# Performance work log

Hardware: AMD Instinct MI355X
Metric: run time of the kernel (lower is better)

## Reference

```python
import jax, jax.numpy as jnp
import numpy as np

B, D_IN, C, P = 8192, 2048, 1000, 256


def setup_inputs() -> dict:
    key = jax.random.key(0)
    ks = jax.random.split(key, 6)
    return {
        "x": jax.random.normal(ks[0], (B, D_IN), dtype=jnp.float32),
        "Wm": jax.random.normal(ks[1], (C, D_IN), dtype=jnp.float32) * (1.0 / np.sqrt(D_IN)),
        "bm": jax.random.normal(ks[2], (C,), dtype=jnp.float32) * 0.01,
        "u": jax.random.normal(ks[3], (P, C), dtype=jnp.float32),
        "v": jax.random.normal(ks[4], (P, C), dtype=jnp.float32),
        "w": jax.random.normal(ks[5], (P, 1), dtype=jnp.float32),
    }


def reference(x, Wm, bm, u, v, w):
    # Backbone: Linear(D_IN -> C) producing per-instance logits (B, C)
    preds = jnp.einsum("bd,cd->bc", x, Wm) + bm
    # Gated attention, fully batched (replaces per-instance Python loop):
    # tanh(u @ pred) * sigmoid(v @ pred)  -> (B, P)
    gated = jnp.tanh(jnp.einsum("bc,pc->bp", preds, u)) * jax.nn.sigmoid(
        jnp.einsum("bc,pc->bp", preds, v)
    )
    scores = (gated @ w).ravel()          # (B,)
    attention = jax.nn.softmax(scores)    # softmax over instances
    total_pred = jnp.sum(preds * attention[:, None])
    return preds, total_pred
```

## Files before the change

### kernel.cpp

```cpp
#include <hip/hip_runtime.h>
#include <hip/hip_fp16.h>

typedef _Float16 half8 __attribute__((ext_vector_type(8)));
typedef float f32x4 __attribute__((ext_vector_type(4)));

#define B_   8192
#define DIN  2048
#define C_   1000
#define CP   1024
#define NP2  512

static const size_t OFF_XH  = 0;
static const size_t OFF_WH  = OFF_XH  + (size_t)B_ * DIN * 2;
static const size_t OFF_UVH = OFF_WH  + (size_t)CP * DIN * 2;
static const size_t OFF_PH  = OFF_UVH + (size_t)NP2 * CP * 2;
static const size_t OFF_SC  = OFF_PH  + (size_t)B_ * CP * 2;
static const size_t OFF_RS  = OFF_SC  + (size_t)B_ * 4;
static const size_t WS_NEED = OFF_RS  + (size_t)B_ * 4;

#define FENCE asm volatile("" ::: "memory")
#define BARRIER do { FENCE; __builtin_amdgcn_s_barrier(); FENCE; } while (0)
#define VMCNT(n) asm volatile("s_waitcnt vmcnt(" #n ")" ::: "memory")
#define PRIO1 __builtin_amdgcn_s_setprio(1)
#define PRIO0 __builtin_amdgcn_s_setprio(0)

__device__ __forceinline__ void gload16(const void* g, void* l) {
  __builtin_amdgcn_global_load_lds(
      (const __attribute__((address_space(1))) void*)g,
      (__attribute__((address_space(3))) void*)l, 16, 0, 0);
}

__global__ __launch_bounds__(256) void prep_kernel(
    const float* __restrict__ x, const float* __restrict__ Wm,
    const float* __restrict__ u, const float* __restrict__ v,
    _Float16* __restrict__ xh, _Float16* __restrict__ wh,
    _Float16* __restrict__ uvh, float* __restrict__ scores,
    float* __restrict__ rowsum)
{
  const long NX  = (long)B_ * DIN / 8;
  const long NW  = (long)CP * DIN / 8;
  const long NUV = (long)NP2 * CP / 8;
  const long NZ  = 2 * (long)B_ / 8;
  const long T   = NX + NW + NUV + NZ;
  for (long idx = (long)blockIdx.x * blockDim.x + threadIdx.x; idx < T;
       idx += (long)gridDim.x * blockDim.x) {
    if (idx < NX) {
      long e = idx * 8;
      float4 p0 = *(const float4*)(x + e);
      float4 p1 = *(const float4*)(x + e + 4);
      half8 h;
      h[0] = (_Float16)p0.x; h[1] = (_Float16)p0.y; h[2] = (_Float16)p0.z; h[3] = (_Float16)p0.w;
      h[4] = (_Float16)p1.x; h[5] = (_Float16)p1.y; h[6] = (_Float16)p1.z; h[7] = (_Float16)p1.w;
      *(half8*)(xh + e) = h;
    } else if (idx < NX + NW) {
      long e = (idx - NX) * 8;
      int row = (int)(e >> 11);
      half8 h;
      if (row < C_) {
        float4 p0 = *(const float4*)(Wm + e);
        float4 p1 = *(const float4*)(Wm + e + 4);
        h[0] = (_Float16)p0.x; h[1] = (_Float16)p0.y; h[2] = (_Float16)p0.z; h[3] = (_Float16)p0.w;
        h[4] = (_Float16)p1.x; h[5] = (_Float16)p1.y; h[6] = (_Float16)p1.z; h[7] = (_Float16)p1.w;
      } else {
        h = (half8)(_Float16)0.f;
      }
      *(half8*)(wh + e) = h;
    } else if (idx < NX + NW + NUV) {
      long e = (idx - NX - NW) * 8;
      int j = (int)(e >> 10);
      int k = (int)(e & 1023);
      const float* src = (j & 1) ? v : u;
      int p = j >> 1;
      half8 h;
      #pragma unroll
      for (int t = 0; t < 8; ++t) {
        int kk = k + t;
        h[t] = (kk < C_) ? (_Float16)src[(size_t)p * C_ + kk] : (_Float16)0.f;
      }
      *(half8*)(uvh + e) = h;
    } else {
      long e = (idx - NX - NW - NUV) * 8;
      float4 z = {0.f, 0.f, 0.f, 0.f};
      if (e < B_) {
        *(float4*)(scores + e) = z; *(float4*)(scores + e + 4) = z;
      } else {
        long r = e - B_;
        *(float4*)(rowsum + r) = z; *(float4*)(rowsum + r + 4) = z;
      }
    }
  }
}

__global__ __launch_bounds__(256, 1) void gemm1_kernel(
    const _Float16* __restrict__ xh, const _Float16* __restrict__ wh,
    const float* __restrict__ bmv, float* __restrict__ preds,
    _Float16* __restrict__ predsh, float* __restrict__ rowsum)
{
  __shared__ _Float16 lds[(3 * 32768 + 3 * 16384) / 2];
  char* const LB = (char*)lds;
  const int tid  = threadIdx.x;
  const int lane = tid & 63;
  const int w    = tid >> 6;
  const int wm   = w >> 1;
  const int wn   = w & 1;
  const int bm0  = blockIdx.x * 256;
  const int bn0  = blockIdx.y * 128;

  f32x4 acc[8][4] = {};

  const int trow = tid >> 3;
  const int swzc = (((tid & 7) << 4) ^ ((trow & 7) << 4)) >> 1;
  const _Float16* pA = xh + (size_t)(bm0 + trow) * DIN + swzc;
  const _Float16* pB = wh + (size_t)(bn0 + trow) * DIN + swzc;

  int aoff[8][2], boff[4][2];
  #pragma unroll
  for (int m = 0; m < 8; ++m)
    #pragma unroll
    for (int ks = 0; ks < 2; ++ks) {
      int ra = wm * 128 + m * 16 + (lane & 15);
      int kb = ks * 64 + (lane >> 4) * 16;
      aoff[m][ks] = ra * 128 + (kb ^ ((ra & 7) << 4));
    }
  #pragma unroll
  for (int n = 0; n < 4; ++n)
    #pragma unroll
    for (int ks = 0; ks < 2; ++ks) {
      int rb = wn * 64 + n * 16 + (lane & 15);
      int kb = ks * 64 + (lane >> 4) * 16;
      boff[n][ks] = rb * 128 + (kb ^ ((rb & 7) << 4));
    }

  half8 A[8][2], Bf[4][2];

  auto stA = [&](int c, int k) {
    gload16(pA + (size_t)k * 32 * DIN, LB + c * 32768 + k * 4096 + w * 1024);
  };
  auto stB = [&](int c, int k) {
    gload16(pB + (size_t)k * 32 * DIN, LB + 98304 + c * 16384 + k * 4096 + w * 1024);
  };
  auto advance = [&]() { pA += 64; pB += 64; };

  auto rdAL = [&](int c) {
    const char* b = LB + c * 32768;
    #pragma unroll
    for (int m = 0; m < 4; ++m)
      #pragma unroll
      for (int ks = 0; ks < 2; ++ks)
        A[m][ks] = *(const half8*)(b + aoff[m][ks]);
  };
  auto rdAH = [&](int c) {
    const char* b = LB + c * 32768;
    #pragma unroll
    for (int m = 4; m < 8; ++m)
      #pragma unroll
      for (int ks = 0; ks < 2; ++ks)
        A[m][ks] = *(const half8*)(b + aoff[m][ks]);
  };
  auto rdBL = [&](int c) {
    const char* b = LB + 98304 + c * 16384;
    #pragma unroll
    for (int n = 0; n < 2; ++n)
      #pragma unroll
      for (int ks = 0; ks < 2; ++ks)
        Bf[n][ks] = *(const half8*)(b + boff[n][ks]);
  };
  auto rdBH = [&](int c) {
    const char* b = LB + 98304 + c * 16384;
    #pragma unroll
    for (int n = 2; n < 4; ++n)
      #pragma unroll
      for (int ks = 0; ks < 2; ++ks)
        Bf[n][ks] = *(const half8*)(b + boff[n][ks]);
  };
  auto mfALBL = [&]() {
    #pragma unroll
    for (int m = 0; m < 4; ++m)
      #pragma unroll
      for (int n = 0; n < 2; ++n)
        #pragma unroll
        for (int ks = 0; ks < 2; ++ks)
          acc[m][n] = __builtin_amdgcn_mfma_f32_16x16x32_f16(A[m][ks], Bf[n][ks], acc[m][n], 0, 0, 0);
  };
  auto mfAHBL = [&]() {
    #pragma unroll
    for (int m = 4; m < 8; ++m)
      #pragma unroll
      for (int n = 0; n < 2; ++n)
        #pragma unroll
        for (int ks = 0; ks < 2; ++ks)
          acc[m][n] = __builtin_amdgcn_mfma_f32_16x16x32_f16(A[m][ks], Bf[n][ks], acc[m][n], 0, 0, 0);
  };
  auto mfALBH = [&]() {
    #pragma unroll
    for (int m = 0; m < 4; ++m)
      #pragma unroll
      for (int n = 2; n < 4; ++n)
        #pragma unroll
        for (int ks = 0; ks < 2; ++ks)
          acc[m][n] = __builtin_amdgcn_mfma_f32_16x16x32_f16(A[m][ks], Bf[n][ks], acc[m][n], 0, 0, 0);
  };
  auto mfAHBH = [&]() {
    #pragma unroll
    for (int m = 4; m < 8; ++m)
      #pragma unroll
      for (int n = 2; n < 4; ++n)
        #pragma unroll
        for (int ks = 0; ks < 2; ++ks)
          acc[m][n] = __builtin_amdgcn_mfma_f32_16x16x32_f16(A[m][ks], Bf[n][ks], acc[m][n], 0, 0, 0);
  };

  #pragma unroll
  for (int k = 0; k < 8; ++k) stA(0, k);
  #pragma unroll
  for (int k = 0; k < 4; ++k) stB(0, k);
  advance();
  #pragma unroll
  for (int k = 0; k < 8; ++k) stA(1, k);
  #pragma unroll
  for (int k = 0; k < 4; ++k) stB(1, k);
  advance();
  VMCNT(12);
  BARRIER;
  rdAL(0); rdBL(0);

  int c0 = 0;
  #pragma unroll 1
  for (int t = 0; t < 30; ++t) {
    const int c1 = (c0 == 2) ? 0 : c0 + 1;
    const int c2 = (c1 == 2) ? 0 : c1 + 1;

    rdAH(c0);
    stA(c2, 0); stA(c2, 1); stA(c2, 2);
    BARRIER;
    PRIO1; mfALBL(); PRIO0;

    rdBH(c0);
    stA(c2, 3); stA(c2, 4); stA(c2, 5);
    VMCNT(6);
    BARRIER;
    PRIO1; mfAHBL(); PRIO0;

    rdBL(c1);
    stA(c2, 6); stA(c2, 7); stB(c2, 0);
    BARRIER;
    PRIO1; mfALBH(); PRIO0;

    rdAL(c1);
    stB(c2, 1); stB(c2, 2); stB(c2, 3);
    advance();
    BARRIER;
    PRIO1; mfAHBH(); PRIO0;

    c0 = c1;
  }

  {
    rdAH(0);
    BARRIER;
    PRIO1; mfALBL(); PRIO0;
    rdBH(0);
    VMCNT(0);
    BARRIER;
    PRIO1; mfAHBL(); PRIO0;
    rdBL(1);
    BARRIER;
    PRIO1; mfALBH(); PRIO0;
    rdAL(1);
    BARRIER;
    PRIO1; mfAHBH(); PRIO0;
    rdAH(1); rdBH(1);
    mfALBL(); mfAHBL(); mfALBH(); mfAHBH();
  }

  float rp[8][4] = {};
  #pragma unroll
  for (int m = 0; m < 8; ++m) {
    #pragma unroll
    for (int n = 0; n < 4; ++n) {
      f32x4 d = acc[m][n];
      int gc = bn0 + wn * 64 + n * 16 + (lane & 15);
      float bias = (gc < C_) ? bmv[gc] : 0.f;
      #pragma unroll
      for (int j = 0; j < 4; ++j) {
        int gr = bm0 + wm * 128 + m * 16 + (lane >> 4) * 4 + j;
        float val = d[j] + bias;
        predsh[(size_t)gr * CP + gc] = (_Float16)val;
        if (gc < C_) preds[(size_t)gr * C_ + gc] = val;
        rp[m][j] += val;
      }
    }
  }
  #pragma unroll
  for (int m = 0; m < 8; ++m) {
    #pragma unroll
    for (int j = 0; j < 4; ++j) {
      float s = rp[m][j];
      s += __shfl_xor(s, 1); s += __shfl_xor(s, 2);
      s += __shfl_xor(s, 4); s += __shfl_xor(s, 8);
      if ((lane & 15) == 0) {
        int gr = bm0 + wm * 128 + m * 16 + (lane >> 4) * 4 + j;
        atomicAdd(&rowsum[gr], s);
      }
    }
  }
}

__global__ __launch_bounds__(256, 1) void gemm2_kernel(
    const _Float16* __restrict__ predsh, const _Float16* __restrict__ uvh,
    const float* __restrict__ wv, float* __restrict__ scores)
{
  __shared__ _Float16 lds2[(3 * 16384 + 3 * 16384) / 2];
  char* const LB = (char*)lds2;
  const int tid  = threadIdx.x;
  const int lane = tid & 63;
  const int w    = tid >> 6;
  const int wm   = w >> 1, wn = w & 1;
  const int bm0  = blockIdx.x * 128;
  const int bn0  = blockIdx.y * 128;

  f32x4 acc[4][4] = {};

  const int trow = tid >> 3;
  const int swzc = (((tid & 7) << 4) ^ ((trow & 7) << 4)) >> 1;
  const _Float16* pA = predsh + (size_t)(bm0 + trow) * CP + swzc;
  const _Float16* pB = uvh    + (size_t)(bn0 + trow) * CP + swzc;

  int aoff[4][2], boff[4][2];
  #pragma unroll
  for (int m = 0; m < 4; ++m)
    #pragma unroll
    for (int ks = 0; ks < 2; ++ks) {
      int ra = wm * 64 + m * 16 + (lane & 15);
      int kb = ks * 64 + (lane >> 4) * 16;
      aoff[m][ks] = ra * 128 + (kb ^ ((ra & 7) << 4));
    }
  #pragma unroll
  for (int n = 0; n < 4; ++n)
    #pragma unroll
    for (int ks = 0; ks < 2; ++ks) {
      int rb = wn * 64 + n * 16 + (lane & 15);
      int kb = ks * 64 + (lane >> 4) * 16;
      boff[n][ks] = rb * 128 + (kb ^ ((rb & 7) << 4));
    }

  half8 A[4][2], Bf[4][2];

  auto stA = [&](int c, int k) {
    gload16(pA + (size_t)k * 32 * CP, LB + c * 16384 + k * 4096 + w * 1024);
  };
  auto stB = [&](int c, int k) {
    gload16(pB + (size_t)k * 32 * CP, LB + 49152 + c * 16384 + k * 4096 + w * 1024);
  };
  auto advance = [&]() { pA += 64; pB += 64; };

  auto rdAL = [&](int c) {
    const char* b = LB + c * 16384;
    #pragma unroll
    for (int m = 0; m < 2; ++m)
      #pragma unroll
      for (int ks = 0; ks < 2; ++ks)
        A[m][ks] = *(const half8*)(b + aoff[m][ks]);
  };
  auto rdAH = [&](int c) {
    const char* b = LB + c * 16384;
    #pragma unroll
    for (int m = 2; m < 4; ++m)
      #pragma unroll
      for (int ks = 0; ks < 2; ++ks)
        A[m][ks] = *(const half8*)(b + aoff[m][ks]);
  };
  auto rdBL = [&](int c) {
    const char* b = LB + 49152 + c * 16384;
    #pragma unroll
    for (int n = 0; n < 2; ++n)
      #pragma unroll
      for (int ks = 0; ks < 2; ++ks)
        Bf[n][ks] = *(const half8*)(b + boff[n][ks]);
  };
  auto rdBH = [&](int c) {
    const char* b = LB + 49152 + c * 16384;
    #pragma unroll
    for (int n = 2; n < 4; ++n)
      #pragma unroll
      for (int ks = 0; ks < 2; ++ks)
        Bf[n][ks] = *(const half8*)(b + boff[n][ks]);
  };
  auto mf = [&](int mlo, int nlo) {
    #pragma unroll
    for (int m = 0; m < 2; ++m)
      #pragma unroll
      for (int n = 0; n < 2; ++n)
        #pragma unroll
        for (int ks = 0; ks < 2; ++ks)
          acc[mlo + m][nlo + n] = __builtin_amdgcn_mfma_f32_16x16x32_f16(
              A[mlo + m][ks], Bf[nlo + n][ks], acc[mlo + m][nlo + n], 0, 0, 0);
  };

  #pragma unroll
  for (int k = 0; k < 4; ++k) stA(0, k);
  #pragma unroll
  for (int k = 0; k < 4; ++k) stB(0, k);
  advance();
  #pragma unroll
  for (int k = 0; k < 4; ++k) stA(1, k);
  #pragma unroll
  for (int k = 0; k < 4; ++k) stB(1, k);
  advance();
  VMCNT(8);
  BARRIER;
  rdAL(0); rdBL(0);

  int c0 = 0;
  #pragma unroll 1
  for (int t = 0; t < 14; ++t) {
    const int c1 = (c0 == 2) ? 0 : c0 + 1;
    const int c2 = (c1 == 2) ? 0 : c1 + 1;

    rdAH(c0);  stA(c2, 0); stA(c2, 1);
    BARRIER;
    PRIO1; mf(0, 0); PRIO0;

    rdBH(c0);  stA(c2, 2); stA(c2, 3);
    VMCNT(4);
    BARRIER;
    PRIO1; mf(2, 0); PRIO0;

    rdBL(c1);  stB(c2, 0); stB(c2, 1);
    BARRIER;
    PRIO1; mf(0, 2); PRIO0;

    rdAL(c1);  stB(c2, 2); stB(c2, 3);
    advance();
    BARRIER;
    PRIO1; mf(2, 2); PRIO0;

    c0 = c1;
  }
  {
    const int c0t = 2, c1t = 0;
    rdAH(c0t);
    BARRIER;
    PRIO1; mf(0, 0); PRIO0;
    rdBH(c0t);
    VMCNT(0);
    BARRIER;
    PRIO1; mf(2, 0); PRIO0;
    rdBL(c1t);
    BARRIER;
    PRIO1; mf(0, 2); PRIO0;
    rdAL(c1t);
    BARRIER;
    PRIO1; mf(2, 2); PRIO0;
    rdAH(c1t); rdBH(c1t);
    mf(0, 0); mf(2, 0); mf(0, 2); mf(2, 2);
  }

  float sp[4][4] = {};
  #pragma unroll
  for (int mi = 0; mi < 4; ++mi) {
    #pragma unroll
    for (int ni = 0; ni < 4; ++ni) {
      f32x4 d = acc[mi][ni];
      int gc = bn0 + wn * 64 + ni * 16 + (lane & 15);
      float wq = wv[gc >> 1];
      bool even = ((gc & 1) == 0);
      #pragma unroll
      for (int j = 0; j < 4; ++j) {
        float t  = d[j];
        float pr = __shfl_xor(t, 1);
        float th = 2.f / (1.f + __expf(-2.f * t)) - 1.f;
        float sg = 1.f / (1.f + __expf(-pr));
        sp[mi][j] += even ? (th * sg * wq) : 0.f;
      }
    }
  }
  #pragma unroll
  for (int mi = 0; mi < 4; ++mi) {
    #pragma unroll
    for (int j = 0; j < 4; ++j) {
      float s = sp[mi][j];
      s += __shfl_xor(s, 1); s += __shfl_xor(s, 2);
      s += __shfl_xor(s, 4); s += __shfl_xor(s, 8);
      if ((lane & 15) == 0) {
        int gr = bm0 + wm * 64 + mi * 16 + (lane >> 4) * 4 + j;
        atomicAdd(&scores[gr], s);
      }
    }
  }
}

__global__ __launch_bounds__(1024) void final_kernel(
    const float* __restrict__ scores, const float* __restrict__ rowsum,
    float* __restrict__ out)
{
  __shared__ float red[16], red2[16];
  const int t = threadIdx.x;
  const int lane = t & 63, wid = t >> 6;
  float s[8];
  float m = -3.4e38f;
  #pragma unroll
  for (int i = 0; i < 8; ++i) { s[i] = scores[t + i * 1024]; m = fmaxf(m, s[i]); }
  #pragma unroll
  for (int off = 1; off < 64; off <<= 1) m = fmaxf(m, __shfl_xor(m, off));
  if (lane == 0) red[wid] = m;
  __syncthreads();
  #pragma unroll
  for (int i = 0; i < 16; ++i) m = fmaxf(m, red[i]);
  __syncthreads();

  float se = 0.f, sr = 0.f;
  #pragma unroll
  for (int i = 0; i < 8; ++i) {
    float e = __expf(s[i] - m);
    se += e;
    sr += e * rowsum[t + i * 1024];
  }
  #pragma unroll
  for (int off = 1; off < 64; off <<= 1) { se += __shfl_xor(se, off); sr += __shfl_xor(sr, off); }
  if (lane == 0) { red[wid] = se; red2[wid] = sr; }
  __syncthreads();
  if (t == 0) {
    float tse = 0.f, tsr = 0.f;
    for (int i = 0; i < 16; ++i) { tse += red[i]; tsr += red2[i]; }
    out[0] = tsr / tse;
  }
}

extern "C" void kernel_launch(void* const* d_in, const int* in_sizes, int n_in,
                              void* d_out, int out_size, void* d_ws, size_t ws_size,
                              hipStream_t stream)
{
  const float* x   = (const float*)d_in[0];
  const float* Wm  = (const float*)d_in[1];
  const float* bmv = (const float*)d_in[2];
  const float* u   = (const float*)d_in[3];
  const float* v   = (const float*)d_in[4];
  const float* wv  = (const float*)d_in[5];
  float* out = (float*)d_out;

  if (ws_size < WS_NEED) return;

  char* ws = (char*)d_ws;
  _Float16* xh     = (_Float16*)(ws + OFF_XH);
  _Float16* wh     = (_Float16*)(ws + OFF_WH);
  _Float16* uvh    = (_Float16*)(ws + OFF_UVH);
  _Float16* predsh = (_Float16*)(ws + OFF_PH);
  float*    scores = (float*)(ws + OFF_SC);
  float*    rowsum = (float*)(ws + OFF_RS);

  prep_kernel<<<2048, 256, 0, stream>>>(x, Wm, u, v, xh, wh, uvh, scores, rowsum);
  gemm1_kernel<<<dim3(32, 8), 256, 0, stream>>>(xh, wh, bmv, out, predsh, rowsum);
  gemm2_kernel<<<dim3(64, 4), 256, 0, stream>>>(predsh, uvh, wv, scores);
  final_kernel<<<1, 1024, 0, stream>>>(scores, rowsum, out + (size_t)B_ * C_);
}
```

Measured before the change: 103.1 us.

## Use 8-wave blocks with ping-pong fragment registers in first GEMM

The first GEMM kernel moves from 4 waves per block to 8 waves on the same 256x128 output tile, so each wave now owns a 64x64 sub-tile. The four-phase split of LDS reads and MFMAs is replaced by whole-stage global loads and two alternating register fragment sets. Fragments for the next K step are read from LDS while the MFMAs run on the current set, with two barriers per K step instead of four. The aim is better latency hiding and less per-wave register pressure, at the cost of more waves contending for LDS bandwidth and coarser load staging.

```diff
diff --git a/kernel.cpp b/kernel.cpp
--- a/kernel.cpp
+++ b/kernel.cpp
@@ -91,7 +91,7 @@
   }
 }
 
-__global__ __launch_bounds__(256, 1) void gemm1_kernel(
+__global__ __launch_bounds__(512, 2) void gemm1_kernel(
     const _Float16* __restrict__ xh, const _Float16* __restrict__ wh,
     const float* __restrict__ bmv, float* __restrict__ preds,
     _Float16* __restrict__ predsh, float* __restrict__ rowsum)
@@ -106,19 +106,19 @@
   const int bm0  = blockIdx.x * 256;
   const int bn0  = blockIdx.y * 128;
 
-  f32x4 acc[8][4] = {};
+  f32x4 acc[4][4] = {};
 
   const int trow = tid >> 3;
   const int swzc = (((tid & 7) << 4) ^ ((trow & 7) << 4)) >> 1;
   const _Float16* pA = xh + (size_t)(bm0 + trow) * DIN + swzc;
   const _Float16* pB = wh + (size_t)(bn0 + trow) * DIN + swzc;
 
-  int aoff[8][2], boff[4][2];
-  #pragma unroll
-  for (int m = 0; m < 8; ++m)
+  int aoff[4][2], boff[4][2];
+  #pragma unroll
+  for (int m = 0; m < 4; ++m)
     #pragma unroll
     for (int ks = 0; ks < 2; ++ks) {
-      int ra = wm * 128 + m * 16 + (lane & 15);
+      int ra = wm * 64 + m * 16 + (lane & 15);
       int kb = ks * 64 + (lane >> 4) * 16;
       aoff[m][ks] = ra * 128 + (kb ^ ((ra & 7) << 4));
     }
@@ -131,151 +131,81 @@
       boff[n][ks] = rb * 128 + (kb ^ ((rb & 7) << 4));
     }
 
-  half8 A[8][2], Bf[4][2];
-
-  auto stA = [&](int c, int k) {
-    gload16(pA + (size_t)k * 32 * DIN, LB + c * 32768 + k * 4096 + w * 1024);
-  };
-  auto stB = [&](int c, int k) {
-    gload16(pB + (size_t)k * 32 * DIN, LB + 98304 + c * 16384 + k * 4096 + w * 1024);
-  };
-  auto advance = [&]() { pA += 64; pB += 64; };
-
-  auto rdAL = [&](int c) {
-    const char* b = LB + c * 32768;
+  half8 Aa[4][2], Ba[4][2], Ab[4][2], Bb[4][2];
+
+  auto stage = [&](int c) {
+    #pragma unroll
+    for (int k = 0; k < 4; ++k)
+      gload16(pA + (size_t)k * 64 * DIN, LB + c * 32768 + k * 8192 + w * 1024);
+    #pragma unroll
+    for (int k = 0; k < 2; ++k)
+      gload16(pB + (size_t)k * 64 * DIN, LB + 98304 + c * 16384 + k * 8192 + w * 1024);
+    pA += 64; pB += 64;
+  };
+  auto rdFrag = [&](int c, half8 (&A)[4][2], half8 (&Bf)[4][2]) {
+    const char* ab = LB + c * 32768;
+    const char* bb = LB + 98304 + c * 16384;
     #pragma unroll
     for (int m = 0; m < 4; ++m)
       #pragma unroll
       for (int ks = 0; ks < 2; ++ks)
-        A[m][ks] = *(const half8*)(b + aoff[m][ks]);
-  };
-  auto rdAH = [&](int c) {
-    const char* b = LB + c * 32768;
-    #pragma unroll
-    for (int m = 4; m < 8; ++m)
-      #pragma unroll
-      for (int ks = 0; ks < 2; ++ks)
-        A[m][ks] = *(const half8*)(b + aoff[m][ks]);
-  };
-  auto rdBL = [&](int c) {
-    const char* b = LB + 98304 + c * 16384;
-    #pragma unroll
-    for (int n = 0; n < 2; ++n)
-      #pragma unroll
-      for (int ks = 0; ks < 2; ++ks)
-        Bf[n][ks] = *(const half8*)(b + boff[n][ks]);
-  };
-  auto rdBH = [&](int c) {
-    const char* b = LB + 98304 + c * 16384;
-    #pragma unroll
-    for (int n = 2; n < 4; ++n)
-      #pragma unroll
-      for (int ks = 0; ks < 2; ++ks)
-        Bf[n][ks] = *(const half8*)(b + boff[n][ks]);
-  };
-  auto mfALBL = [&]() {
+        A[m][ks] = *(const half8*)(ab + aoff[m][ks]);
+    #pragma unroll
+    for (int n = 0; n < 4; ++n)
+      #pragma unroll
+      for (int ks = 0; ks < 2; ++ks)
+        Bf[n][ks] = *(const half8*)(bb + boff[n][ks]);
+  };
+  auto mfAll = [&](half8 (&A)[4][2], half8 (&Bf)[4][2]) {
+    PRIO1;
     #pragma unroll
     for (int m = 0; m < 4; ++m)
       #pragma unroll
-      for (int n = 0; n < 2; ++n)
+      for (int n = 0; n < 4; ++n)
         #pragma unroll
         for (int ks = 0; ks < 2; ++ks)
           acc[m][n] = __builtin_amdgcn_mfma_f32_16x16x32_f16(A[m][ks], Bf[n][ks], acc[m][n], 0, 0, 0);
-  };
-  auto mfAHBL = [&]() {
-    #pragma unroll
-    for (int m = 4; m < 8; ++m)
-      #pragma unroll
-      for (int n = 0; n < 2; ++n)
-        #pragma unroll
-        for (int ks = 0; ks < 2; ++ks)
-          acc[m][n] = __builtin_amdgcn_mfma_f32_16x16x32_f16(A[m][ks], Bf[n][ks], acc[m][n], 0, 0, 0);
-  };
-  auto mfALBH = [&]() {
-    #pragma unroll
-    for (int m = 0; m < 4; ++m)
-      #pragma unroll
-      for (int n = 2; n < 4; ++n)
-        #pragma unroll
-        for (int ks = 0; ks < 2; ++ks)
-          acc[m][n] = __builtin_amdgcn_mfma_f32_16x16x32_f16(A[m][ks], Bf[n][ks], acc[m][n], 0, 0, 0);
-  };
-  auto mfAHBH = [&]() {
-    #pragma unroll
-    for (int m = 4; m < 8; ++m)
-      #pragma unroll
-      for (int n = 2; n < 4; ++n)
-        #pragma unroll
-        for (int ks = 0; ks < 2; ++ks)
-          acc[m][n] = __builtin_amdgcn_mfma_f32_16x16x32_f16(A[m][ks], Bf[n][ks], acc[m][n], 0, 0, 0);
-  };
-
-  #pragma unroll
-  for (int k = 0; k < 8; ++k) stA(0, k);
-  #pragma unroll
-  for (int k = 0; k < 4; ++k) stB(0, k);
-  advance();
-  #pragma unroll
-  for (int k = 0; k < 8; ++k) stA(1, k);
-  #pragma unroll
-  for (int k = 0; k < 4; ++k) stB(1, k);
-  advance();
-  VMCNT(12);
+    PRIO0;
+  };
+
+  stage(0);
+  stage(1);
+  VMCNT(6);
   BARRIER;
-  rdAL(0); rdBL(0);
+  rdFrag(0, Aa, Ba);
 
   int c0 = 0;
   #pragma unroll 1
-  for (int t = 0; t < 30; ++t) {
+  for (int t = 0; t < 30; t += 2) {
     const int c1 = (c0 == 2) ? 0 : c0 + 1;
     const int c2 = (c1 == 2) ? 0 : c1 + 1;
 
-    rdAH(c0);
-    stA(c2, 0); stA(c2, 1); stA(c2, 2);
-    BARRIER;
-    PRIO1; mfALBL(); PRIO0;
-
-    rdBH(c0);
-    stA(c2, 3); stA(c2, 4); stA(c2, 5);
+    stage(c2);
     VMCNT(6);
     BARRIER;
-    PRIO1; mfAHBL(); PRIO0;
-
-    rdBL(c1);
-    stA(c2, 6); stA(c2, 7); stB(c2, 0);
-    BARRIER;
-    PRIO1; mfALBH(); PRIO0;
-
-    rdAL(c1);
-    stB(c2, 1); stB(c2, 2); stB(c2, 3);
-    advance();
-    BARRIER;
-    PRIO1; mfAHBH(); PRIO0;
-
-    c0 = c1;
-  }
-
-  {
-    rdAH(0);
-    BARRIER;
-    PRIO1; mfALBL(); PRIO0;
-    rdBH(0);
-    VMCNT(0);
-    BARRIER;
-    PRIO1; mfAHBL(); PRIO0;
-    rdBL(1);
-    BARRIER;
-    PRIO1; mfALBH(); PRIO0;
-    rdAL(1);
-    BARRIER;
-    PRIO1; mfAHBH(); PRIO0;
-    rdAH(1); rdBH(1);
-    mfALBL(); mfAHBL(); mfALBH(); mfAHBH();
-  }
-
-  float rp[8][4] = {};
-  #pragma unroll
-  for (int m = 0; m < 8; ++m) {
+    rdFrag(c1, Ab, Bb);
+    mfAll(Aa, Ba);
+    BARRIER;
+
+    stage(c0);
+    VMCNT(6);
+    BARRIER;
+    rdFrag(c2, Aa, Ba);
+    mfAll(Ab, Bb);
+    BARRIER;
+
+    c0 = c2;
+  }
+
+  VMCNT(0);
+  BARRIER;
+  rdFrag(1, Ab, Bb);
+  mfAll(Aa, Ba);
+  mfAll(Ab, Bb);
+
+  float rp[4][4] = {};
+  #pragma unroll
+  for (int m = 0; m < 4; ++m) {
     #pragma unroll
     for (int n = 0; n < 4; ++n) {
       f32x4 d = acc[m][n];
@@ -283,7 +213,7 @@
       float bias = (gc < C_) ? bmv[gc] : 0.f;
       #pragma unroll
       for (int j = 0; j < 4; ++j) {
-        int gr = bm0 + wm * 128 + m * 16 + (lane >> 4) * 4 + j;
+        int gr = bm0 + wm * 64 + m * 16 + (lane >> 4) * 4 + j;
         float val = d[j] + bias;
         predsh[(size_t)gr * CP + gc] = (_Float16)val;
         if (gc < C_) preds[(size_t)gr * C_ + gc] = val;
@@ -292,14 +222,14 @@
     }
   }
   #pragma unroll
-  for (int m = 0; m < 8; ++m) {
+  for (int m = 0; m < 4; ++m) {
     #pragma unroll
     for (int j = 0; j < 4; ++j) {
       float s = rp[m][j];
       s += __shfl_xor(s, 1); s += __shfl_xor(s, 2);
       s += __shfl_xor(s, 4); s += __shfl_xor(s, 8);
       if ((lane & 15) == 0) {
-        int gr = bm0 + wm * 128 + m * 16 + (lane >> 4) * 4 + j;
+        int gr = bm0 + wm * 64 + m * 16 + (lane >> 4) * 4 + j;
         atomicAdd(&rowsum[gr], s);
       }
     }
@@ -550,7 +480,7 @@
   float*    rowsum = (float*)(ws + OFF_RS);
 
   prep_kernel<<<2048, 256, 0, stream>>>(x, Wm, u, v, xh, wh, uvh, scores, rowsum);
-  gemm1_kernel<<<dim3(32, 8), 256, 0, stream>>>(xh, wh, bmv, out, predsh, rowsum);
+  gemm1_kernel<<<dim3(32, 8), 512, 0, stream>>>(xh, wh, bmv, out, predsh, rowsum);
   gemm2_kernel<<<dim3(64, 4), 256, 0, stream>>>(predsh, uvh, wv, scores);
   final_kernel<<<1, 1024, 0, stream>>>(scores, rowsum, out + (size_t)B_ * C_);
 }
```

New measurement: 94.86 us. -8.0%, faster.
